# Performance work log

Hardware: AMD Instinct MI355X
Metric: run time of the kernel (lower is better)

The kernel has to match this reference:

```python
import jax, jax.numpy as jnp
import numpy as np
import math

HASHMAP_SIZE = 1 << 17
N_LEVELS = 16
N_FEATURES = 2
BASE_RES = 16.0
GROWTH = 1.5  # per-level resolution growth factor
PRIME_Y = np.uint32(2654435761)  # Instant-NGP spatial hash prime


def hash_encode(x, encoding):
    """Multiresolution 2D hash-grid encoding with bilinear interpolation.
    x: [N, 2] in [0,1); encoding: [T, L, F]. Returns [N, L*F]."""
    N = x.shape[0]
    scales = jnp.asarray(BASE_RES * GROWTH ** np.arange(N_LEVELS),
                         dtype=x.dtype)  # [L]
    pos = x[:, None, :] * scales[None, :, None]        # [N, L, 2]
    pf = jnp.floor(pos)
    frac = pos - pf                                    # [N, L, 2]
    pi = pf.astype(jnp.uint32)                         # integer corner base
    lvl = jnp.arange(N_LEVELS)[None, :]                # [1, L]

    feat = jnp.zeros((N, N_LEVELS, N_FEATURES), dtype=x.dtype)
    for cx in (0, 1):
        for cy in (0, 1):
            ix = pi[..., 0] + jnp.uint32(cx)
            iy = pi[..., 1] + jnp.uint32(cy)
            h = ix ^ (iy * PRIME_Y)                    # spatial hash (wraps mod 2^32)
            idx = (h & jnp.uint32(HASHMAP_SIZE - 1)).astype(jnp.int32)  # [N, L]
            wx = frac[..., 0] if cx else 1.0 - frac[..., 0]
            wy = frac[..., 1] if cy else 1.0 - frac[..., 1]
            feat = feat + (wx * wy)[..., None] * encoding[idx, lvl]  # gather [N,L,F]
    return feat.reshape(N, N_LEVELS * N_FEATURES)


def setup_inputs() -> dict:
    key = jax.random.key(0)
    ks = jax.random.split(key, 8)
    N = 1 << 20
    n_neurons = [32, 64, 64, 3]
    x = jax.random.uniform(ks[0], (N, 2), dtype=jnp.float32)
    # encoding init: rand * 2e-4 - 1e-4
    encoding = jax.random.uniform(ks[1], (HASHMAP_SIZE, N_LEVELS, N_FEATURES),
                                  dtype=jnp.float32) * 2e-4 - 1e-4
    inp = {"x": x, "encoding": encoding}
    for i in range(3):
        s = 1.0 / math.sqrt(n_neurons[i])
        w = jax.random.uniform(ks[2 + i], (n_neurons[i], n_neurons[i + 1]),
                               dtype=jnp.float32) * 2 * s - s
        b = jax.random.uniform(ks[5 + i], (n_neurons[i + 1],),
                               dtype=jnp.float32) * 2 * s - s
        inp[f"w{i}"] = w
        inp[f"b{i}"] = b
    return inp


def reference(x, encoding, w0, b0, w1, b1, w2, b2):
    feat = hash_encode(x, encoding)                 # [N, 32]
    h = jax.nn.relu(feat @ w0 + b0)                 # [N, 64]
    h = jax.nn.relu(h @ w1 + b1)                    # [N, 64]
    return h @ w2 + b2                              # [N, 3]
```

## Files before the change

kernel.cpp:

```cpp
#include <hip/hip_runtime.h>
#include <stdint.h>

typedef __bf16 bf16_t;
typedef bf16_t bf16x8 __attribute__((ext_vector_type(8)));
typedef float  f32x4  __attribute__((ext_vector_type(4)));
typedef float  f32x2v __attribute__((ext_vector_type(2)));

static constexpr uint32_t PRIME = 2654435761u;
static constexpr uint32_t HMASK = (1u << 17) - 1u;
static constexpr uint32_t TSIZE = 1u << 17;

static constexpr int NLDS   = 5308;
static constexpr int NDALL  = 136642;

static constexpr float FSCALE = 8192.0f;
static constexpr float WSCALE = 1.0f / 8192.0f;

__device__ __forceinline__ uint32_t fbits(float f) {
    union { float f; uint32_t u; } v; v.f = f; return v.u;
}
__device__ __forceinline__ float asfloat(uint32_t u) {
    union { uint32_t u; float f; } v; v.u = u; return v.f;
}

__device__ __forceinline__ uint32_t enc8(float v) {
    const uint32_t s = (fbits(v) >> 24) & 0x80u;
    float m = fabsf(v) * 0x1p-120f;
    uint32_t u = fbits(m);
    u += 0x7FFFFu + ((u >> 20) & 1u);
    return s | ((u >> 20) & 0x7fu);
}
__device__ __forceinline__ uint32_t pack8(float a, float b) {
#if __has_builtin(__builtin_amdgcn_cvt_pk_fp8_f32)
    return (uint32_t)__builtin_amdgcn_cvt_pk_fp8_f32(a, b, 0, false) & 0xffffu;
#else
    return enc8(a) | (enc8(b) << 8);
#endif
}
__device__ __forceinline__ float2 unpack8(uint32_t u) {
#if __has_builtin(__builtin_amdgcn_cvt_pk_f32_fp8)
    f32x2v r = __builtin_amdgcn_cvt_pk_f32_fp8((int)u, false);
    return make_float2(r.x, r.y);
#else
    const float f0 = asfloat(((u & 0x80u) << 24) | ((u & 0x7fu) << 20)) * 0x1p120f;
    const float f1 = asfloat(((u & 0x8000u) << 16) | ((u & 0x7f00u) << 12)) * 0x1p120f;
    return make_float2(f0, f1);
#endif
}

__global__ __launch_bounds__(256)
void repack_enc8(const float2* __restrict__ src, uint16_t* __restrict__ dst) {
    __shared__ uint16_t ldsT[8 * 257];
    const int tid = threadIdx.x;
    const int t0  = blockIdx.x * 256;
#pragma unroll
    for (int k = 0; k < 8; ++k) {
        const int j = k * 256 + tid;
        const int tl = j >> 3, l8 = j & 7;
        const float2 f = src[((size_t)(t0 + tl) << 4) + 8 + l8];
        ldsT[l8 * 257 + tl] = (uint16_t)pack8(f.x * FSCALE, f.y * FSCALE);
    }
    __syncthreads();
#pragma unroll
    for (int k = 0; k < 8; ++k)
        dst[((uint32_t)k << 17) + t0 + tid] = ldsT[k * 257 + tid];
}

__global__ __launch_bounds__(256)
void densify_enc(const float2* __restrict__ src, uint16_t* __restrict__ dst) {
    const int i = blockIdx.x * 256 + threadIdx.x;
    if (i >= NDALL) return;
    int lvl, W, off;
    if      (i <   289) { lvl = 0; W =  17; off = 0;     }
    else if (i <   914) { lvl = 1; W =  25; off = 289;   }
    else if (i <  2283) { lvl = 2; W =  37; off = 914;   }
    else if (i <  5308) { lvl = 3; W =  55; off = 2283;  }
    else if (i < 12032) { lvl = 4; W =  82; off = 5308;  }
    else if (i < 27161) { lvl = 5; W = 123; off = 12032; }
    else if (i < 61017) { lvl = 6; W = 184; off = 27161; }
    else                { lvl = 7; W = 275; off = 61017; }
    const int li = i - off;
    const uint32_t iy = (uint32_t)(li / W), ix = (uint32_t)(li % W);
    const uint32_t h = (ix ^ (iy * PRIME)) & HMASK;
    const float2 f = src[h * 16 + lvl];
    dst[i] = (uint16_t)pack8(f.x * FSCALE, f.y * FSCALE);
}

__global__ __launch_bounds__(256, 2)
void fused_hash_mlp(const float* __restrict__ xin,
                    const uint16_t* __restrict__ tab8,
                    const uint16_t* __restrict__ dense,
                    const float* __restrict__ w0, const float* __restrict__ b0,
                    const float* __restrict__ w1, const float* __restrict__ b1,
                    const float* __restrict__ w2, const float* __restrict__ b2,
                    float* __restrict__ out,
                    int nGroups)
{
    __shared__ uint16_t ldsTab[NLDS];
    __shared__ __align__(16) bf16_t lds[4 * 16 * 80];

    const int tid  = threadIdx.x;
    const int wib  = tid >> 6;
    const int lane = tid & 63;
    const int q    = lane >> 4;
    const int n16  = lane & 15;

    bf16_t* myLds = &lds[wib * (16 * 80)];

    for (int i = tid; i < NLDS; i += 256) ldsTab[i] = dense[i];

    bf16x8 Bw0[4], Bw1[2][4], Bw2[2];
#pragma unroll
    for (int t = 0; t < 4; ++t)
#pragma unroll
        for (int j = 0; j < 8; ++j)
            Bw0[t][j] = (bf16_t)(w0[(q * 8 + j) * 64 + t * 16 + n16] * WSCALE);
#pragma unroll
    for (int c = 0; c < 2; ++c)
#pragma unroll
        for (int t = 0; t < 4; ++t)
#pragma unroll
            for (int j = 0; j < 8; ++j)
                Bw1[c][t][j] = (bf16_t)w1[(c * 32 + q * 8 + j) * 64 + t * 16 + n16];
#pragma unroll
    for (int c = 0; c < 2; ++c)
#pragma unroll
        for (int j = 0; j < 8; ++j)
            Bw2[c][j] = (n16 < 3) ? (bf16_t)w2[(c * 32 + q * 8 + j) * 3 + n16]
                                  : (bf16_t)0.0f;

    float bv0[4], bv1[4];
#pragma unroll
    for (int t = 0; t < 4; ++t) {
        bv0[t] = b0[t * 16 + n16];
        bv1[t] = b1[t * 16 + n16];
    }
    const float bv2 = (n16 < 3) ? b2[n16] : 0.0f;

    const float sb = 16.0f * ((q == 0) ? 1.0f :
                              (q == 1) ? 5.0625f :
                              (q == 2) ? 25.62890625f :
                                         129.746337890625f);
    const float sc[4] = { sb, sb * 1.5f, sb * 2.25f, sb * 3.375f };

    const uint32_t l8base = ((uint32_t)((q >= 2 ? q - 2 : 0) * 4)) << 17;

    __syncthreads();

    for (int g = blockIdx.x; g < nGroups; g += gridDim.x) {
        const int tile = g * 4 + wib;
        const int p = tile * 16 + n16;
        const float2 xy = ((const float2*)xin)[p];
        const float px = xy.x, py = xy.y;

        bf16x8 af;
#pragma unroll
        for (int lv = 0; lv < 4; ++lv) {
            const float posx = px * sc[lv], posy = py * sc[lv];
            const float fx = floorf(posx), fy = floorf(posy);
            const float frx = posx - fx,  fry = posy - fy;
            const uint32_t ix = (uint32_t)fx, iy = (uint32_t)fy;

            const uint32_t Wl = (lv == 0) ? 17u  : (lv == 1) ? 25u
                              : (lv == 2) ? 37u  : 55u;
            const uint32_t Ol = (lv == 0) ? 0u   : (lv == 1) ? 289u
                              : (lv == 2) ? 914u : 2283u;
            const uint32_t Wg = (lv == 0) ? 82u    : (lv == 1) ? 123u
                              : (lv == 2) ? 184u   : 275u;
            const uint32_t Og = (lv == 0) ? 5308u  : (lv == 1) ? 12032u
                              : (lv == 2) ? 27161u : 61017u;

            uint32_t u00, u10, u01, u11;
            if (q == 0) {
                const uint32_t a = Ol + iy * Wl + ix;
                u00 = ldsTab[a];
                u10 = ldsTab[a + 1];
                u01 = ldsTab[a + Wl];
                u11 = ldsTab[a + Wl + 1];
            } else if (q == 1) {
                const uint32_t a = Og + iy * Wg + ix;
                u00 = dense[a];
                u10 = dense[a + 1];
                u01 = dense[a + Wg];
                u11 = dense[a + Wg + 1];
            } else {
                const uint32_t hy0 = iy * PRIME, hy1 = hy0 + PRIME;
                const uint32_t i00 = ( ix       ^ hy0) & HMASK;
                const uint32_t i10 = ((ix + 1u) ^ hy0) & HMASK;
                const uint32_t i01 = ( ix       ^ hy1) & HMASK;
                const uint32_t i11 = ((ix + 1u) ^ hy1) & HMASK;
                const uint32_t base = l8base + ((uint32_t)lv << 17);
                u00 = tab8[base + i00];
                u10 = tab8[base + i10];
                u01 = tab8[base + i01];
                u11 = tab8[base + i11];
            }

            const float2 e00 = unpack8(u00);
            const float2 e10 = unpack8(u10);
            const float2 e01 = unpack8(u01);
            const float2 e11 = unpack8(u11);
            const float wx1 = frx, wx0 = 1.0f - frx, wy1 = fry, wy0 = 1.0f - fry;
            const float w00 = wx0 * wy0, w10 = wx1 * wy0, w01 = wx0 * wy1, w11 = wx1 * wy1;
            const float f0 = w00 * e00.x + w10 * e10.x + w01 * e01.x + w11 * e11.x;
            const float f1 = w00 * e00.y + w10 * e10.y + w01 * e01.y + w11 * e11.y;
            af[2 * lv]     = (bf16_t)f0;
            af[2 * lv + 1] = (bf16_t)f1;
        }

        f32x4 c0[4];
#pragma unroll
        for (int t = 0; t < 4; ++t) {
            f32x4 cc = { bv0[t], bv0[t], bv0[t], bv0[t] };
            c0[t] = __builtin_amdgcn_mfma_f32_16x16x32_bf16(af, Bw0[t], cc, 0, 0, 0);
        }

#pragma unroll
        for (int t = 0; t < 4; ++t)
#pragma unroll
            for (int r = 0; r < 4; ++r)
                myLds[(q * 4 + r) * 80 + t * 16 + n16] = (bf16_t)fmaxf(c0[t][r], 0.0f);

        bf16x8 A1[2];
#pragma unroll
        for (int c = 0; c < 2; ++c)
            A1[c] = *(const bf16x8*)&myLds[n16 * 80 + c * 32 + q * 8];

        f32x4 c1[4];
#pragma unroll
        for (int t = 0; t < 4; ++t) {
            f32x4 cc = { bv1[t], bv1[t], bv1[t], bv1[t] };
            cc    = __builtin_amdgcn_mfma_f32_16x16x32_bf16(A1[0], Bw1[0][t], cc, 0, 0, 0);
            c1[t] = __builtin_amdgcn_mfma_f32_16x16x32_bf16(A1[1], Bw1[1][t], cc, 0, 0, 0);
        }

#pragma unroll
        for (int t = 0; t < 4; ++t)
#pragma unroll
            for (int r = 0; r < 4; ++r)
                myLds[(q * 4 + r) * 80 + t * 16 + n16] = (bf16_t)fmaxf(c1[t][r], 0.0f);

        bf16x8 A2[2];
#pragma unroll
        for (int c = 0; c < 2; ++c)
            A2[c] = *(const bf16x8*)&myLds[n16 * 80 + c * 32 + q * 8];

        f32x4 co = { bv2, bv2, bv2, bv2 };
        co = __builtin_amdgcn_mfma_f32_16x16x32_bf16(A2[0], Bw2[0], co, 0, 0, 0);
        co = __builtin_amdgcn_mfma_f32_16x16x32_bf16(A2[1], Bw2[1], co, 0, 0, 0);

        if (n16 < 3) {
#pragma unroll
            for (int r = 0; r < 4; ++r)
                out[(size_t)(tile * 16 + q * 4 + r) * 3 + n16] = co[r];
        }
    }
}

__global__ __launch_bounds__(256)
void fused_hash_mlp_fp32(const float* __restrict__ xin,
                         const float* __restrict__ enc,
                         const float* __restrict__ w0, const float* __restrict__ b0,
                         const float* __restrict__ w1, const float* __restrict__ b1,
                         const float* __restrict__ w2, const float* __restrict__ b2,
                         float* __restrict__ out,
                         int nGroups)
{
    __shared__ __align__(16) bf16_t lds[4 * 16 * 80];
    const int tid  = threadIdx.x;
    const int wib  = tid >> 6;
    const int lane = tid & 63;
    const int q    = lane >> 4;
    const int n16  = lane & 15;
    bf16_t* myLds = &lds[wib * (16 * 80)];

    bf16x8 Bw0[4], Bw1[2][4], Bw2[2];
#pragma unroll
    for (int t = 0; t < 4; ++t)
#pragma unroll
        for (int j = 0; j < 8; ++j)
            Bw0[t][j] = (bf16_t)w0[(q * 8 + j) * 64 + t * 16 + n16];
#pragma unroll
    for (int c = 0; c < 2; ++c)
#pragma unroll
        for (int t = 0; t < 4; ++t)
#pragma unroll
            for (int j = 0; j < 8; ++j)
                Bw1[c][t][j] = (bf16_t)w1[(c * 32 + q * 8 + j) * 64 + t * 16 + n16];
#pragma unroll
    for (int c = 0; c < 2; ++c)
#pragma unroll
        for (int j = 0; j < 8; ++j)
            Bw2[c][j] = (n16 < 3) ? (bf16_t)w2[(c * 32 + q * 8 + j) * 3 + n16]
                                  : (bf16_t)0.0f;

    float bv0[4], bv1[4];
#pragma unroll
    for (int t = 0; t < 4; ++t) { bv0[t] = b0[t * 16 + n16]; bv1[t] = b1[t * 16 + n16]; }
    const float bv2 = (n16 < 3) ? b2[n16] : 0.0f;

    const float sb = 16.0f * ((q == 0) ? 1.0f : (q == 1) ? 5.0625f :
                              (q == 2) ? 25.62890625f : 129.746337890625f);
    const float sc[4] = { sb, sb * 1.5f, sb * 2.25f, sb * 3.375f };
    const char* encB = (const char*)enc;
    const uint32_t lvBase = (uint32_t)q * 32u;

    for (int g = blockIdx.x; g < nGroups; g += gridDim.x) {
        const int tile = g * 4 + wib;
        const int p = tile * 16 + n16;
        const float2 xy = ((const float2*)xin)[p];
        const float px = xy.x, py = xy.y;

        bf16x8 af;
#pragma unroll
        for (int lv = 0; lv < 4; ++lv) {
            const float posx = px * sc[lv], posy = py * sc[lv];
            const float fx = floorf(posx), fy = floorf(posy);
            const float frx = posx - fx,  fry = posy - fy;
            const uint32_t ix = (uint32_t)fx, iy = (uint32_t)fy;
            const uint32_t hy0 = iy * PRIME, hy1 = hy0 + PRIME;
            const uint32_t i00 = ( ix       ^ hy0) & HMASK;
            const uint32_t i10 = ((ix + 1u) ^ hy0) & HMASK;
            const uint32_t i01 = ( ix       ^ hy1) & HMASK;
            const uint32_t i11 = ((ix + 1u) ^ hy1) & HMASK;
            const uint32_t off = lvBase + (uint32_t)lv * 8u;
            const float2 e00 = *(const float2*)(encB + (i00 * 128u + off));
            const float2 e10 = *(const float2*)(encB + (i10 * 128u + off));
            const float2 e01 = *(const float2*)(encB + (i01 * 128u + off));
            const float2 e11 = *(const float2*)(encB + (i11 * 128u + off));
            const float wx1 = frx, wx0 = 1.0f - frx, wy1 = fry, wy0 = 1.0f - fry;
            const float w00 = wx0 * wy0, w10 = wx1 * wy0, w01 = wx0 * wy1, w11 = wx1 * wy1;
            af[2 * lv]     = (bf16_t)(w00 * e00.x + w10 * e10.x + w01 * e01.x + w11 * e11.x);
            af[2 * lv + 1] = (bf16_t)(w00 * e00.y + w10 * e10.y + w01 * e01.y + w11 * e11.y);
        }

        f32x4 c0[4];
#pragma unroll
        for (int t = 0; t < 4; ++t) {
            f32x4 cc = { bv0[t], bv0[t], bv0[t], bv0[t] };
            c0[t] = __builtin_amdgcn_mfma_f32_16x16x32_bf16(af, Bw0[t], cc, 0, 0, 0);
        }
        __syncthreads();
#pragma unroll
        for (int t = 0; t < 4; ++t)
#pragma unroll
            for (int r = 0; r < 4; ++r)
                myLds[(q * 4 + r) * 80 + t * 16 + n16] = (bf16_t)fmaxf(c0[t][r], 0.0f);
        __syncthreads();
        bf16x8 A1[2];
#pragma unroll
        for (int c = 0; c < 2; ++c)
            A1[c] = *(const bf16x8*)&myLds[n16 * 80 + c * 32 + q * 8];

        f32x4 c1[4];
#pragma unroll
        for (int t = 0; t < 4; ++t) {
            f32x4 cc = { bv1[t], bv1[t], bv1[t], bv1[t] };
            cc    = __builtin_amdgcn_mfma_f32_16x16x32_bf16(A1[0], Bw1[0][t], cc, 0, 0, 0);
            c1[t] = __builtin_amdgcn_mfma_f32_16x16x32_bf16(A1[1], Bw1[1][t], cc, 0, 0, 0);
        }
        __syncthreads();
#pragma unroll
        for (int t = 0; t < 4; ++t)
#pragma unroll
            for (int r = 0; r < 4; ++r)
                myLds[(q * 4 + r) * 80 + t * 16 + n16] = (bf16_t)fmaxf(c1[t][r], 0.0f);
        __syncthreads();
        bf16x8 A2[2];
#pragma unroll
        for (int c = 0; c < 2; ++c)
            A2[c] = *(const bf16x8*)&myLds[n16 * 80 + c * 32 + q * 8];

        f32x4 co = { bv2, bv2, bv2, bv2 };
        co = __builtin_amdgcn_mfma_f32_16x16x32_bf16(A2[0], Bw2[0], co, 0, 0, 0);
        co = __builtin_amdgcn_mfma_f32_16x16x32_bf16(A2[1], Bw2[1], co, 0, 0, 0);
        if (n16 < 3) {
#pragma unroll
            for (int r = 0; r < 4; ++r)
                out[(size_t)(tile * 16 + q * 4 + r) * 3 + n16] = co[r];
        }
    }
}

extern "C" void kernel_launch(void* const* d_in, const int* in_sizes, int n_in,
                              void* d_out, int out_size, void* d_ws, size_t ws_size,
                              hipStream_t stream) {
    const float* x  = (const float*)d_in[0];
    const float* en = (const float*)d_in[1];
    const float* w0 = (const float*)d_in[2];
    const float* b0 = (const float*)d_in[3];
    const float* w1 = (const float*)d_in[4];
    const float* b1 = (const float*)d_in[5];
    const float* w2 = (const float*)d_in[6];
    const float* b2 = (const float*)d_in[7];
    float* out = (float*)d_out;

    const int N = in_sizes[0] / 2;
    const int nTiles = N / 16;
    const int nGroups = nTiles / 4;

    const size_t wsNeeded = ((size_t)TSIZE * 8 + NDALL) * 2;
    if (ws_size >= wsNeeded) {
        uint16_t* tab8  = (uint16_t*)d_ws;
        uint16_t* dense = tab8 + ((size_t)TSIZE * 8);
        repack_enc8<<<TSIZE / 256, 256, 0, stream>>>((const float2*)en, tab8);
        densify_enc<<<(NDALL + 255) / 256, 256, 0, stream>>>((const float2*)en, dense);
        int blocks = 2048;
        if (blocks > nGroups) blocks = nGroups;
        fused_hash_mlp<<<blocks, 256, 0, stream>>>(x, tab8, dense,
                                                   w0, b0, w1, b1, w2, b2, out, nGroups);
    } else {
        int blocks = 2048;
        if (blocks > nGroups) blocks = nGroups;
        fused_hash_mlp_fp32<<<blocks, 256, 0, stream>>>(x, en, w0, b0, w1, b1, w2, b2, out, nGroups);
    }
}
```

Measured before the change: 201.8 us.

## Merge prepass kernels, pair dense corners, prefetch next tile gathers, swizzle LDS

Measured after the change: 226.9 us. 12.4% more time.

```diff
diff --git a/kernel.cpp b/kernel.cpp
--- a/kernel.cpp
+++ b/kernel.cpp
@@ -10,7 +10,6 @@
 static constexpr uint32_t HMASK = (1u << 17) - 1u;
 static constexpr uint32_t TSIZE = 1u << 17;
 
-static constexpr int NLDS   = 5308;
 static constexpr int NDALL  = 136642;
 
 static constexpr float FSCALE = 8192.0f;
@@ -37,77 +36,82 @@
     return enc8(a) | (enc8(b) << 8);
 #endif
 }
-__device__ __forceinline__ float2 unpack8(uint32_t u) {
+template <bool HI>
+__device__ __forceinline__ float2 unpack8w(uint32_t u) {
 #if __has_builtin(__builtin_amdgcn_cvt_pk_f32_fp8)
-    f32x2v r = __builtin_amdgcn_cvt_pk_f32_fp8((int)u, false);
+    f32x2v r = __builtin_amdgcn_cvt_pk_f32_fp8((int)u, HI);
     return make_float2(r.x, r.y);
 #else
-    const float f0 = asfloat(((u & 0x80u) << 24) | ((u & 0x7fu) << 20)) * 0x1p120f;
-    const float f1 = asfloat(((u & 0x8000u) << 16) | ((u & 0x7f00u) << 12)) * 0x1p120f;
+    const uint32_t w = HI ? (u >> 16) : (u & 0xffffu);
+    const float f0 = asfloat(((w & 0x80u) << 24) | ((w & 0x7fu) << 20)) * 0x1p120f;
+    const float f1 = asfloat(((w & 0x8000u) << 16) | ((w & 0x7f00u) << 12)) * 0x1p120f;
     return make_float2(f0, f1);
 #endif
 }
 
 __global__ __launch_bounds__(256)
-void repack_enc8(const float2* __restrict__ src, uint16_t* __restrict__ dst) {
+void prepass_all(const float2* __restrict__ src, uint16_t* __restrict__ tab8,
+                 uint32_t* __restrict__ dpair) {
     __shared__ uint16_t ldsT[8 * 257];
     const int tid = threadIdx.x;
-    const int t0  = blockIdx.x * 256;
-#pragma unroll
-    for (int k = 0; k < 8; ++k) {
-        const int j = k * 256 + tid;
-        const int tl = j >> 3, l8 = j & 7;
-        const float2 f = src[((size_t)(t0 + tl) << 4) + 8 + l8];
-        ldsT[l8 * 257 + tl] = (uint16_t)pack8(f.x * FSCALE, f.y * FSCALE);
+    if (blockIdx.x < 512) {
+        const int t0 = blockIdx.x * 256;
+#pragma unroll
+        for (int k = 0; k < 8; ++k) {
+            const int j = k * 256 + tid;
+            const int tl = j >> 3, l8 = j & 7;
+            const float2 f = src[((size_t)(t0 + tl) << 4) + 8 + l8];
+            ldsT[l8 * 257 + tl] = (uint16_t)pack8(f.x * FSCALE, f.y * FSCALE);
+        }
+        __syncthreads();
+#pragma unroll
+        for (int k = 0; k < 8; ++k)
+            tab8[((uint32_t)k << 17) + t0 + tid] = ldsT[k * 257 + tid];
+    } else {
+        const int i = (blockIdx.x - 512) * 256 + tid;
+        if (i >= NDALL) return;
+        int lvl, W, off;
+        if      (i <   289) { lvl = 0; W =  17; off = 0;     }
+        else if (i <   914) { lvl = 1; W =  25; off = 289;   }
+        else if (i <  2283) { lvl = 2; W =  37; off = 914;   }
+        else if (i <  5308) { lvl = 3; W =  55; off = 2283;  }
+        else if (i < 12032) { lvl = 4; W =  82; off = 5308;  }
+        else if (i < 27161) { lvl = 5; W = 123; off = 12032; }
+        else if (i < 61017) { lvl = 6; W = 184; off = 27161; }
+        else                { lvl = 7; W = 275; off = 61017; }
+        const int li = i - off;
+        const uint32_t iy = (uint32_t)(li / W), ix = (uint32_t)(li % W);
+        const uint32_t hy = iy * PRIME;
+        const uint32_t h0 = ( ix       ^ hy) & HMASK;
+        const uint32_t h1 = ((ix + 1u) ^ hy) & HMASK;
+        const float2 f0 = src[h0 * 16 + lvl];
+        const float2 f1 = src[h1 * 16 + lvl];
+        dpair[i] = pack8(f0.x * FSCALE, f0.y * FSCALE)
+                 | (pack8(f1.x * FSCALE, f1.y * FSCALE) << 16);
     }
-    __syncthreads();
-#pragma unroll
-    for (int k = 0; k < 8; ++k)
-        dst[((uint32_t)k << 17) + t0 + tid] = ldsT[k * 257 + tid];
-}
-
-__global__ __launch_bounds__(256)
-void densify_enc(const float2* __restrict__ src, uint16_t* __restrict__ dst) {
-    const int i = blockIdx.x * 256 + threadIdx.x;
-    if (i >= NDALL) return;
-    int lvl, W, off;
-    if      (i <   289) { lvl = 0; W =  17; off = 0;     }
-    else if (i <   914) { lvl = 1; W =  25; off = 289;   }
-    else if (i <  2283) { lvl = 2; W =  37; off = 914;   }
-    else if (i <  5308) { lvl = 3; W =  55; off = 2283;  }
-    else if (i < 12032) { lvl = 4; W =  82; off = 5308;  }
-    else if (i < 27161) { lvl = 5; W = 123; off = 12032; }
-    else if (i < 61017) { lvl = 6; W = 184; off = 27161; }
-    else                { lvl = 7; W = 275; off = 61017; }
-    const int li = i - off;
-    const uint32_t iy = (uint32_t)(li / W), ix = (uint32_t)(li % W);
-    const uint32_t h = (ix ^ (iy * PRIME)) & HMASK;
-    const float2 f = src[h * 16 + lvl];
-    dst[i] = (uint16_t)pack8(f.x * FSCALE, f.y * FSCALE);
 }
 
 __global__ __launch_bounds__(256, 2)
 void fused_hash_mlp(const float* __restrict__ xin,
                     const uint16_t* __restrict__ tab8,
-                    const uint16_t* __restrict__ dense,
+                    const uint32_t* __restrict__ dpair,
                     const float* __restrict__ w0, const float* __restrict__ b0,
                     const float* __restrict__ w1, const float* __restrict__ b1,
                     const float* __restrict__ w2, const float* __restrict__ b2,
                     float* __restrict__ out,
                     int nGroups)
 {
-    __shared__ uint16_t ldsTab[NLDS];
-    __shared__ __align__(16) bf16_t lds[4 * 16 * 80];
+    __shared__ __align__(16) bf16_t lds[4 * 16 * 64];
 
     const int tid  = threadIdx.x;
     const int wib  = tid >> 6;
     const int lane = tid & 63;
     const int q    = lane >> 4;
     const int n16  = lane & 15;
-
-    bf16_t* myLds = &lds[wib * (16 * 80)];
-
-    for (int i = tid; i < NLDS; i += 256) ldsTab[i] = dense[i];
+    const int m7   = n16 & 7;
+    const int mb   = n16 >> 3;
+
+    bf16_t* myLds = &lds[wib * (16 * 64)];
 
     bf16x8 Bw0[4], Bw1[2][4], Bw2[2];
 #pragma unroll
@@ -145,22 +149,26 @@
 
     const uint32_t l8base = ((uint32_t)((q >= 2 ? q - 2 : 0) * 4)) << 17;
 
-    __syncthreads();
-
-    for (int g = blockIdx.x; g < nGroups; g += gridDim.x) {
-        const int tile = g * 4 + wib;
-        const int p = tile * 16 + n16;
-        const float2 xy = ((const float2*)xin)[p];
-        const float px = xy.x, py = xy.y;
-
-        bf16x8 af;
-#pragma unroll
-        for (int lv = 0; lv < 4; ++lv) {
-            const float posx = px * sc[lv], posy = py * sc[lv];
-            const float fx = floorf(posx), fy = floorf(posy);
-            const float frx = posx - fx,  fry = posy - fy;
-            const uint32_t ix = (uint32_t)fx, iy = (uint32_t)fy;
-
+    int wbase[4];
+#pragma unroll
+    for (int r = 0; r < 4; ++r)
+        wbase[r] = (q * 4 + r) * 64 + m7 + ((mb ^ (r & 1)) << 3) + ((q & 1) << 5);
+    const int rIdx0 = n16 * 64 + (( q      ^ m7) << 3);
+    const int rIdx1 = n16 * 64 + (((4 + q) ^ m7) << 3);
+
+    const int gstride = gridDim.x;
+    const int gLast   = nGroups - 1;
+
+    auto ldxy = [&](int gg) -> float2 {
+        return ((const float2*)xin)[(gg * 4 + wib) * 16 + n16];
+    };
+
+    uint32_t u[4][4] = { {0,0,0,0}, {0,0,0,0}, {0,0,0,0}, {0,0,0,0} };
+
+    auto prefetchLvl = [&](float px, float py, int lv) {
+        const float posx = px * sc[lv], posy = py * sc[lv];
+        const uint32_t ix = (uint32_t)posx, iy = (uint32_t)posy;
+        if (q < 2) {
             const uint32_t Wl = (lv == 0) ? 17u  : (lv == 1) ? 25u
                               : (lv == 2) ? 37u  : 55u;
             const uint32_t Ol = (lv == 0) ? 0u   : (lv == 1) ? 289u
@@ -169,43 +177,55 @@
                               : (lv == 2) ? 184u   : 275u;
             const uint32_t Og = (lv == 0) ? 5308u  : (lv == 1) ? 12032u
                               : (lv == 2) ? 27161u : 61017u;
-
-            uint32_t u00, u10, u01, u11;
-            if (q == 0) {
-                const uint32_t a = Ol + iy * Wl + ix;
-                u00 = ldsTab[a];
-                u10 = ldsTab[a + 1];
-                u01 = ldsTab[a + Wl];
-                u11 = ldsTab[a + Wl + 1];
-            } else if (q == 1) {
-                const uint32_t a = Og + iy * Wg + ix;
-                u00 = dense[a];
-                u10 = dense[a + 1];
-                u01 = dense[a + Wg];
-                u11 = dense[a + Wg + 1];
+            const uint32_t W = (q == 0) ? Wl : Wg;
+            const uint32_t O = (q == 0) ? Ol : Og;
+            const uint32_t a = O + iy * W + ix;
+            u[lv][0] = dpair[a];
+            u[lv][1] = dpair[a + W];
+        } else {
+            const uint32_t hy0 = iy * PRIME, hy1 = hy0 + PRIME;
+            const uint32_t base = l8base + ((uint32_t)lv << 17);
+            u[lv][0] = tab8[base + (( ix       ^ hy0) & HMASK)];
+            u[lv][2] = tab8[base + (((ix + 1u) ^ hy0) & HMASK)];
+            u[lv][1] = tab8[base + (( ix       ^ hy1) & HMASK)];
+            u[lv][3] = tab8[base + (((ix + 1u) ^ hy1) & HMASK)];
+        }
+    };
+
+    int g = blockIdx.x;
+    if (g > gLast) return;
+
+    float2 xyA = ldxy(g);
+#pragma unroll
+    for (int lv = 0; lv < 4; ++lv) prefetchLvl(xyA.x, xyA.y, lv);
+    int g1 = g + gstride; if (g1 > gLast) g1 = gLast;
+    float2 xyB = ldxy(g1);
+
+    for (; g <= gLast; g += gstride) {
+        int gC = g + 2 * gstride; if (gC > gLast) gC = gLast;
+        const float2 xyC = ldxy(gC);
+
+        bf16x8 af;
+#pragma unroll
+        for (int lv = 0; lv < 4; ++lv) {
+            const float posx = xyA.x * sc[lv], posy = xyA.y * sc[lv];
+            const float frx = posx - floorf(posx), fry = posy - floorf(posy);
+            float2 e00, e10, e01, e11;
+            if (q < 2) {
+                e00 = unpack8w<false>(u[lv][0]); e10 = unpack8w<true>(u[lv][0]);
+                e01 = unpack8w<false>(u[lv][1]); e11 = unpack8w<true>(u[lv][1]);
             } else {
-                const uint32_t hy0 = iy * PRIME, hy1 = hy0 + PRIME;
-                const uint32_t i00 = ( ix       ^ hy0) & HMASK;
-                const uint32_t i10 = ((ix + 1u) ^ hy0) & HMASK;
-                const uint32_t i01 = ( ix       ^ hy1) & HMASK;
-                const uint32_t i11 = ((ix + 1u) ^ hy1) & HMASK;
-                const uint32_t base = l8base + ((uint32_t)lv << 17);
-                u00 = tab8[base + i00];
-                u10 = tab8[base + i10];
-                u01 = tab8[base + i01];
-                u11 = tab8[base + i11];
+                e00 = unpack8w<false>(u[lv][0]); e10 = unpack8w<false>(u[lv][2]);
+                e01 = unpack8w<false>(u[lv][1]); e11 = unpack8w<false>(u[lv][3]);
             }
-
-            const float2 e00 = unpack8(u00);
-            const float2 e10 = unpack8(u10);
-            const float2 e01 = unpack8(u01);
-            const float2 e11 = unpack8(u11);
             const float wx1 = frx, wx0 = 1.0f - frx, wy1 = fry, wy0 = 1.0f - fry;
-            const float w00 = wx0 * wy0, w10 = wx1 * wy0, w01 = wx0 * wy1, w11 = wx1 * wy1;
+            const float w00 = wx0 * wy0, w10 = wx1 * wy0;
+            const float w01 = wx0 * wy1, w11 = wx1 * wy1;
             const float f0 = w00 * e00.x + w10 * e10.x + w01 * e01.x + w11 * e11.x;
             const float f1 = w00 * e00.y + w10 * e10.y + w01 * e01.y + w11 * e11.y;
             af[2 * lv]     = (bf16_t)f0;
             af[2 * lv + 1] = (bf16_t)f1;
+            prefetchLvl(xyB.x, xyB.y, lv);
         }
 
         f32x4 c0[4];
@@ -218,13 +238,14 @@
 #pragma unroll
         for (int t = 0; t < 4; ++t)
 #pragma unroll
-            for (int r = 0; r < 4; ++r)
-                myLds[(q * 4 + r) * 80 + t * 16 + n16] = (bf16_t)fmaxf(c0[t][r], 0.0f);
-
+            for (int r = 0; r < 4; ++r) {
+                const int idx = ((t < 2) ? wbase[r] : (wbase[r] ^ 32))
+                              + ((((t & 1) ^ ((r >> 1) & 1))) << 4);
+                myLds[idx] = (bf16_t)fmaxf(c0[t][r], 0.0f);
+            }
         bf16x8 A1[2];
-#pragma unroll
-        for (int c = 0; c < 2; ++c)
-            A1[c] = *(const bf16x8*)&myLds[n16 * 80 + c * 32 + q * 8];
+        A1[0] = *(const bf16x8*)&myLds[rIdx0];
+        A1[1] = *(const bf16x8*)&myLds[rIdx1];
 
         f32x4 c1[4];
 #pragma unroll
@@ -237,23 +258,27 @@
 #pragma unroll
         for (int t = 0; t < 4; ++t)
 #pragma unroll
-            for (int r = 0; r < 4; ++r)
-                myLds[(q * 4 + r) * 80 + t * 16 + n16] = (bf16_t)fmaxf(c1[t][r], 0.0f);
-
+            for (int r = 0; r < 4; ++r) {
+                const int idx = ((t < 2) ? wbase[r] : (wbase[r] ^ 32))
+                              + ((((t & 1) ^ ((r >> 1) & 1))) << 4);
+                myLds[idx] = (bf16_t)fmaxf(c1[t][r], 0.0f);
+            }
         bf16x8 A2[2];
-#pragma unroll
-        for (int c = 0; c < 2; ++c)
-            A2[c] = *(const bf16x8*)&myLds[n16 * 80 + c * 32 + q * 8];
+        A2[0] = *(const bf16x8*)&myLds[rIdx0];
+        A2[1] = *(const bf16x8*)&myLds[rIdx1];
 
         f32x4 co = { bv2, bv2, bv2, bv2 };
         co = __builtin_amdgcn_mfma_f32_16x16x32_bf16(A2[0], Bw2[0], co, 0, 0, 0);
         co = __builtin_amdgcn_mfma_f32_16x16x32_bf16(A2[1], Bw2[1], co, 0, 0, 0);
 
+        const int tile = g * 4 + wib;
         if (n16 < 3) {
 #pragma unroll
             for (int r = 0; r < 4; ++r)
                 out[(size_t)(tile * 16 + q * 4 + r) * 3 + n16] = co[r];
         }
+
+        xyA = xyB; xyB = xyC;
     }
 }
 
@@ -399,15 +424,16 @@
     const int nTiles = N / 16;
     const int nGroups = nTiles / 4;
 
-    const size_t wsNeeded = ((size_t)TSIZE * 8 + NDALL) * 2;
+    const size_t tabBytes = (size_t)TSIZE * 8 * 2;
+    const size_t wsNeeded = tabBytes + (size_t)NDALL * 4;
     if (ws_size >= wsNeeded) {
         uint16_t* tab8  = (uint16_t*)d_ws;
-        uint16_t* dense = tab8 + ((size_t)TSIZE * 8);
-        repack_enc8<<<TSIZE / 256, 256, 0, stream>>>((const float2*)en, tab8);
-        densify_enc<<<(NDALL + 255) / 256, 256, 0, stream>>>((const float2*)en, dense);
+        uint32_t* dpair = (uint32_t*)((char*)d_ws + tabBytes);
+        const int preBlocks = 512 + (NDALL + 255) / 256;
+        prepass_all<<<preBlocks, 256, 0, stream>>>((const float2*)en, tab8, dpair);
         int blocks = 2048;
         if (blocks > nGroups) blocks = nGroups;
-        fused_hash_mlp<<<blocks, 256, 0, stream>>>(x, tab8, dense,
+        fused_hash_mlp<<<blocks, 256, 0, stream>>>(x, tab8, dpair,
                                                    w0, b0, w1, b1, w2, b2, out, nGroups);
     } else {
         int blocks = 2048;
```
